# Kernel tuning notes

Hardware: AMD Instinct MI355X
Metric: run time of the kernel (lower is better)

Reference implementation:

```python
import jax, jax.numpy as jnp
import numpy as np

B, L, D = 4, 1024, 1024
N, H = 16, 64
FFW = 4096
LYR = 6
PDIM = 768            # 3 * 16^2
POS_EMB = 64
POOL_K = 4
EPS = 1e-6
BASE = 10000.0
GRID = 32             # 32x32 patch grid


def rms_norm(x, scale=None, eps=EPS):
    v = jnp.mean(jnp.square(x.astype(jnp.float32)), axis=-1, keepdims=True)
    y = (x.astype(jnp.float32) * jax.lax.rsqrt(v + eps)).astype(x.dtype)
    return y * scale if scale is not None else y


def _rope_half(x, pos, base):
    # x: [B, L, N, Hh]; pos: [B, L] int coords
    Hh = x.shape[-1]
    inv = 1.0 / (base ** (jnp.arange(Hh // 2, dtype=jnp.float32) / (Hh // 2)))
    ang = pos.astype(jnp.float32)[..., None] * inv          # [B, L, Hh/2]
    cos = jnp.cos(ang)[:, :, None, :]
    sin = jnp.sin(ang)[:, :, None, :]
    x1, x2 = jnp.split(x, 2, axis=-1)
    return jnp.concatenate([x1 * cos - x2 * sin, x2 * cos + x1 * sin], axis=-1)


def apply_2d_rope(x, px, py, base):
    # first half of head_dim rotated by x-coord, second half by y-coord
    xa, xb = jnp.split(x, 2, axis=-1)
    return jnp.concatenate([_rope_half(xa, px, base), _rope_half(xb, py, base)], axis=-1)


def setup_inputs() -> dict:
    key = jax.random.key(0)
    ks = jax.random.split(key, 12)
    pixel_values = jax.random.uniform(ks[0], (B, L, PDIM), dtype=jnp.float32)
    gx = jnp.arange(L, dtype=jnp.int32) % GRID
    gy = jnp.arange(L, dtype=jnp.int32) // GRID
    position_ids = jnp.broadcast_to(jnp.stack([gx, gy], -1), (B, L, 2))
    s = 0.02
    Win = jax.random.normal(ks[1], (PDIM, D), jnp.float32) * s
    pos_table = jax.random.normal(ks[2], (2, POS_EMB, D), jnp.float32) * s
    Wq = jax.random.normal(ks[3], (LYR, D, N * H), jnp.float32) * s
    Wk = jax.random.normal(ks[4], (LYR, D, N * H), jnp.float32) * s
    Wv = jax.random.normal(ks[5], (LYR, D, N * H), jnp.float32) * s
    Wo = jax.random.normal(ks[6], (LYR, N * H, D), jnp.float32) * s
    Wg = jax.random.normal(ks[7], (LYR, D, FFW), jnp.float32) * s
    Wu = jax.random.normal(ks[8], (LYR, D, FFW), jnp.float32) * s
    Wd = jax.random.normal(ks[9], (LYR, FFW, D), jnp.float32) * s
    qn = jnp.ones((LYR, H), jnp.float32)
    kn = jnp.ones((LYR, H), jnp.float32)
    pre_attn = jnp.ones((LYR, D), jnp.float32)
    post_attn = jnp.ones((LYR, D), jnp.float32)
    pre_ffw = jnp.ones((LYR, D), jnp.float32)
    post_ffw = jnp.ones((LYR, D), jnp.float32)
    return dict(pixel_values=pixel_values, position_ids=position_ids, Win=Win,
                pos_table=pos_table, Wq=Wq, Wk=Wk, Wv=Wv, Wo=Wo, qn=qn, kn=kn,
                pre_attn=pre_attn, post_attn=post_attn, pre_ffw=pre_ffw,
                post_ffw=post_ffw, Wg=Wg, Wu=Wu, Wd=Wd)


def _encoder(pixel_values, position_ids, Win, pos_table, Wq, Wk, Wv, Wo, qn, kn,
             pre_attn, post_attn, pre_ffw, post_ffw, Wg, Wu, Wd):
    padding = jnp.all(position_ids == -1, axis=-1)          # [B, L] True = pad
    valid = ~padding
    big_neg = jnp.finfo(jnp.float32).min
    amask = jnp.where((valid[:, :, None] & valid[:, None, :])[:, None], 0.0, big_neg)  # [B,1,L,L]

    px = position_ids[:, :, 0]
    py = position_ids[:, :, 1]
    clamped = jnp.maximum(position_ids, 0)

    # patch embed
    pix = 2.0 * (pixel_values - 0.5)
    x = pix @ Win
    pos_emb = pos_table[0][clamped[..., 0]] + pos_table[1][clamped[..., 1]]
    x = x + jnp.where(padding[..., None], 0.0, pos_emb)

    for i in range(LYR):
        # attention
        res = x
        h = rms_norm(x, pre_attn[i])
        q = (h @ Wq[i]).reshape(B, L, N, H)
        k = (h @ Wk[i]).reshape(B, L, N, H)
        v = (h @ Wv[i]).reshape(B, L, N, H)
        q = rms_norm(q, qn[i])
        k = rms_norm(k, kn[i])
        v = rms_norm(v)                                     # with_scale=False
        q = apply_2d_rope(q, px, py, BASE)
        k = apply_2d_rope(k, px, py, BASE)
        scores = jnp.einsum('bqnh,bknh->bnqk', q, k) + amask  # no 1/sqrt(H), matches source
        w = jax.nn.softmax(scores.astype(jnp.float32), axis=-1).astype(v.dtype)
        o = jnp.einsum('bnqk,bknh->bqnh', w, v).reshape(B, L, N * H) @ Wo[i]
        x = res + rms_norm(o, post_attn[i])
        # GeGLU MLP
        res = x
        h = rms_norm(x, pre_ffw[i])
        m = (jax.nn.gelu(h @ Wg[i], approximate=True) * (h @ Wu[i])) @ Wd[i]
        x = res + rms_norm(m, post_ffw[i])

    # pooler: 4x4 position-based average pooling
    out_len = L // (POOL_K ** 2)
    kk = int((L / out_len) ** 0.5)
    x = jnp.where(padding[..., None], 0.0, x)
    max_x = jnp.max(clamped[..., 0], axis=-1, keepdims=True) + 1   # [B,1]
    kidx = clamped // kk
    kidx = kidx[..., 0] + (max_x // kk) * kidx[..., 1]             # [B, L]
    weights = jax.nn.one_hot(kidx, out_len, dtype=jnp.float32) / (kk * kk)
    pooled = jnp.einsum('blo,bld->bod', weights, x.astype(jnp.float32))
    mask = jnp.any(weights != 0, axis=1)                           # [B, out_len]
    pooled = pooled.astype(x.dtype) * jnp.sqrt(jnp.float32(D))
    pooled = jnp.where(mask[..., None], pooled, 0.0)               # jit-safe stand-in for hidden[mask]
    return pooled, mask


def reference(pixel_values, position_ids, Win, pos_table, Wq, Wk, Wv, Wo, qn, kn,
              pre_attn, post_attn, pre_ffw, post_ffw, Wg, Wu, Wd):
    return _encoder(pixel_values, position_ids, Win, pos_table, Wq, Wk, Wv, Wo,
                    qn, kn, pre_attn, post_attn, pre_ffw, post_ffw, Wg, Wu, Wd)
```

## Files before the change

### kernel.cpp

```cpp
#include <hip/hip_runtime.h>
#include <stdint.h>

typedef unsigned short ushort_t;
using frag8 = __attribute__((ext_vector_type(8))) short;
using f32x4 = __attribute__((ext_vector_type(4))) float;

static __device__ __forceinline__ unsigned short f2bf(float f) {
  union { float f; unsigned u; } v; v.f = f;
  unsigned r = v.u + 0x7fffu + ((v.u >> 16) & 1u);
  return (unsigned short)(r >> 16);
}
static __device__ __forceinline__ float bf2f(unsigned short b) {
  union { unsigned u; float f; } v; v.u = ((unsigned)b) << 16; return v.f;
}
static __device__ __forceinline__ void splitf(float v, ushort_t& h, ushort_t& m) {
  h = f2bf(v);
  m = f2bf(v - bf2f(h));
}

__global__ __launch_bounds__(256) void k_splitpix(const float* __restrict__ pix,
                                                  ushort_t* __restrict__ oh,
                                                  ushort_t* __restrict__ om, int n4) {
  int i = blockIdx.x * 256 + threadIdx.x;
  if (i >= n4) return;
  float4 v = ((const float4*)pix)[i];
  ushort4 h, m;
  splitf(2.f * (v.x - 0.5f), h.x, m.x);
  splitf(2.f * (v.y - 0.5f), h.y, m.y);
  splitf(2.f * (v.z - 0.5f), h.z, m.z);
  splitf(2.f * (v.w - 0.5f), h.w, m.w);
  ((ushort4*)oh)[i] = h;
  ((ushort4*)om)[i] = m;
}

__global__ __launch_bounds__(256) void k_posemb(const int* __restrict__ pos,
                                                const float* __restrict__ ptab,
                                                float* __restrict__ x) {
  int row = blockIdx.x, tid = threadIdx.x;
  int p0 = pos[(size_t)row * 2], p1 = pos[(size_t)row * 2 + 1];
  bool pad = (p0 == -1) && (p1 == -1);
  int px = p0 > 0 ? p0 : 0, py = p1 > 0 ? p1 : 0;
  float4 a = ((const float4*)(ptab + (size_t)px * 1024))[tid];
  float4 b = ((const float4*)(ptab + 65536 + (size_t)py * 1024))[tid];
  float4 o;
  o.x = pad ? 0.f : a.x + b.x;
  o.y = pad ? 0.f : a.y + b.y;
  o.z = pad ? 0.f : a.z + b.z;
  o.w = pad ? 0.f : a.w + b.w;
  ((float4*)(x + (size_t)row * 1024))[tid] = o;
}

__global__ __launch_bounds__(256) void k_rmsnorm_s(const float* __restrict__ x,
                                                   const float* __restrict__ scale,
                                                   ushort_t* __restrict__ oh,
                                                   ushort_t* __restrict__ om) {
  __shared__ float wsum[4];
  int row = blockIdx.x, tid = threadIdx.x;
  float4 v = ((const float4*)(x + (size_t)row * 1024))[tid];
  float ss = v.x * v.x + v.y * v.y + v.z * v.z + v.w * v.w;
  for (int m = 1; m < 64; m <<= 1) ss += __shfl_xor(ss, m);
  if ((tid & 63) == 0) wsum[tid >> 6] = ss;
  __syncthreads();
  float tot = wsum[0] + wsum[1] + wsum[2] + wsum[3];
  float r = rsqrtf(tot * (1.f / 1024.f) + 1e-6f);
  float4 sc = ((const float4*)scale)[tid];
  ushort4 h, m;
  splitf(v.x * r * sc.x, h.x, m.x);
  splitf(v.y * r * sc.y, h.y, m.y);
  splitf(v.z * r * sc.z, h.z, m.z);
  splitf(v.w * r * sc.w, h.w, m.w);
  ((ushort4*)(oh + (size_t)row * 1024))[tid] = h;
  ((ushort4*)(om + (size_t)row * 1024))[tid] = m;
}

__global__ __launch_bounds__(256) void k_addrms32(float* __restrict__ x,
                                                  const float* __restrict__ t,
                                                  const float* __restrict__ scale) {
  __shared__ float wsum[4];
  int row = blockIdx.x, tid = threadIdx.x;
  float4 v = ((const float4*)(t + (size_t)row * 1024))[tid];
  float ss = v.x * v.x + v.y * v.y + v.z * v.z + v.w * v.w;
  for (int m = 1; m < 64; m <<= 1) ss += __shfl_xor(ss, m);
  if ((tid & 63) == 0) wsum[tid >> 6] = ss;
  __syncthreads();
  float tot = wsum[0] + wsum[1] + wsum[2] + wsum[3];
  float r = rsqrtf(tot * (1.f / 1024.f) + 1e-6f);
  float4 sc = ((const float4*)scale)[tid];
  float4 xv = ((const float4*)(x + (size_t)row * 1024))[tid];
  xv.x += v.x * r * sc.x;
  xv.y += v.y * r * sc.y;
  xv.z += v.z * r * sc.z;
  xv.w += v.w * r * sc.w;
  ((float4*)(x + (size_t)row * 1024))[tid] = xv;
}

__global__ __launch_bounds__(256) void k_qkv(const ushort_t* __restrict__ Ah,
                                             const ushort_t* __restrict__ Am,
                                             const float* __restrict__ Wq,
                                             const float* __restrict__ Wk,
                                             const float* __restrict__ Wv,
                                             const float* __restrict__ qn,
                                             const float* __restrict__ kn,
                                             const int* __restrict__ pos,
                                             ushort_t* __restrict__ qh, ushort_t* __restrict__ qm,
                                             ushort_t* __restrict__ kh, ushort_t* __restrict__ km,
                                             ushort_t* __restrict__ vh, ushort_t* __restrict__ vm) {
  __shared__ __align__(16) ushort_t Ash[128][40];
  __shared__ __align__(16) ushort_t Asl[128][40];
  __shared__ __align__(16) ushort_t Bsh[128][40];
  __shared__ __align__(16) ushort_t Bsl[128][40];
  const int tid = threadIdx.x;
  const int bid = blockIdx.x;
  const int xcd = bid & 7, lo = bid >> 3;
  const int ntl = lo % 3, mt = lo / 3;
  const int nt = xcd * 3 + ntl;
  const int mat = nt >> 3;
  const int n0 = (nt & 7) << 7;
  const int m0 = mt << 7;
  const float* B = (mat == 0) ? Wq : (mat == 1 ? Wk : Wv);

  const int lane = tid & 63;
  const int wm = ((tid >> 7) & 1) * 64;
  const int wn = ((tid >> 6) & 1) * 64;
  const int l15 = lane & 15, lg = lane >> 4;
  const int arow = tid >> 1, acol = (tid & 1) << 4;
  const int bnn = tid & 127, bk0 = (tid >> 7) << 4;
  f32x4 acc[4][4] = {};

  for (int k0 = 0; k0 < 1024; k0 += 32) {
    const ushort_t* gah = Ah + (size_t)(m0 + arow) * 1024 + (k0 + acol);
    const ushort_t* gam = Am + (size_t)(m0 + arow) * 1024 + (k0 + acol);
    uint4 a0 = *(const uint4*)gah;
    uint4 a1 = *(const uint4*)(gah + 8);
    uint4 a2 = *(const uint4*)gam;
    uint4 a3 = *(const uint4*)(gam + 8);
    const float* gb = B + (size_t)(k0 + bk0) * 1024 + (n0 + bnn);
    float bv[16];
#pragma unroll
    for (int j = 0; j < 16; ++j) bv[j] = gb[(size_t)j * 1024];
    *(uint4*)(&Ash[arow][acol]) = a0;
    *(uint4*)(&Ash[arow][acol + 8]) = a1;
    *(uint4*)(&Asl[arow][acol]) = a2;
    *(uint4*)(&Asl[arow][acol + 8]) = a3;
#pragma unroll
    for (int g = 0; g < 4; ++g) {
      ushort4 wh, wl;
      splitf(bv[g * 4 + 0], wh.x, wl.x);
      splitf(bv[g * 4 + 1], wh.y, wl.y);
      splitf(bv[g * 4 + 2], wh.z, wl.z);
      splitf(bv[g * 4 + 3], wh.w, wl.w);
      *(ushort4*)(&Bsh[bnn][bk0 + (g << 2)]) = wh;
      *(ushort4*)(&Bsl[bnn][bk0 + (g << 2)]) = wl;
    }
    __syncthreads();
    frag8 ah[4], al[4], bh[4], bl[4];
#pragma unroll
    for (int i = 0; i < 4; ++i) {
      ah[i] = *(const frag8*)(&Ash[wm + i * 16 + l15][lg << 3]);
      al[i] = *(const frag8*)(&Asl[wm + i * 16 + l15][lg << 3]);
      bh[i] = *(const frag8*)(&Bsh[wn + i * 16 + l15][lg << 3]);
      bl[i] = *(const frag8*)(&Bsl[wn + i * 16 + l15][lg << 3]);
    }
#pragma unroll
    for (int mi = 0; mi < 4; ++mi)
#pragma unroll
      for (int ni = 0; ni < 4; ++ni) {
        acc[mi][ni] = __builtin_amdgcn_mfma_f32_16x16x32_bf16(ah[mi], bh[ni], acc[mi][ni], 0, 0, 0);
        acc[mi][ni] = __builtin_amdgcn_mfma_f32_16x16x32_bf16(ah[mi], bl[ni], acc[mi][ni], 0, 0, 0);
        acc[mi][ni] = __builtin_amdgcn_mfma_f32_16x16x32_bf16(al[mi], bh[ni], acc[mi][ni], 0, 0, 0);
      }
    __syncthreads();
  }

  const float* scale = (mat == 0) ? qn : (mat == 1 ? kn : nullptr);
  ushort_t* outh = (mat == 0) ? qh : (mat == 1 ? kh : vh);
  ushort_t* outm = (mat == 0) ? qm : (mat == 1 ? km : vm);
  const float inv = powf(10000.f, -(float)l15 * (1.f / 16.f));
#pragma unroll
  for (int mi = 0; mi < 4; ++mi) {
#pragma unroll
    for (int rr = 0; rr < 4; ++rr) {
      float ss = 0.f;
#pragma unroll
      for (int ni = 0; ni < 4; ++ni) { float v = acc[mi][ni][rr]; ss += v * v; }
      ss += __shfl_xor(ss, 1);
      ss += __shfl_xor(ss, 2);
      ss += __shfl_xor(ss, 4);
      ss += __shfl_xor(ss, 8);
      float rs = rsqrtf(ss * (1.f / 64.f) + 1e-6f);
      int row = m0 + wm + mi * 16 + (lg << 2) + rr;
      float nv[4];
#pragma unroll
      for (int ni = 0; ni < 4; ++ni) {
        float sc = scale ? scale[ni * 16 + l15] : 1.f;
        nv[ni] = acc[mi][ni][rr] * rs * sc;
      }
      if (mat < 2) {
        int p0 = pos[(size_t)row * 2], p1 = pos[(size_t)row * 2 + 1];
        p0 = p0 > 0 ? p0 : 0;
        p1 = p1 > 0 ? p1 : 0;
        float a0 = (float)p0 * inv, a1 = (float)p1 * inv;
        float c0 = cosf(a0), s0 = sinf(a0);
        float c1 = cosf(a1), s1 = sinf(a1);
        float t0 = nv[0] * c0 - nv[1] * s0;
        float t1 = nv[1] * c0 + nv[0] * s0;
        float t2 = nv[2] * c1 - nv[3] * s1;
        float t3 = nv[3] * c1 + nv[2] * s1;
        nv[0] = t0; nv[1] = t1; nv[2] = t2; nv[3] = t3;
      }
#pragma unroll
      for (int ni = 0; ni < 4; ++ni) {
        ushort_t h, m;
        splitf(nv[ni], h, m);
        size_t idx = (size_t)row * 1024 + n0 + wn + ni * 16 + l15;
        outh[idx] = h;
        outm[idx] = m;
      }
    }
  }
}

__global__ __launch_bounds__(256) void k_ffw_up(const ushort_t* __restrict__ Ah,
                                                const ushort_t* __restrict__ Am,
                                                const float* __restrict__ Wg,
                                                const float* __restrict__ Wu,
                                                ushort_t* __restrict__ Oh,
                                                ushort_t* __restrict__ Om) {
  __shared__ __align__(16) ushort_t Ash[128][40];
  __shared__ __align__(16) ushort_t Asl[128][40];
  __shared__ __align__(16) ushort_t Bgh[128][40];
  __shared__ __align__(16) ushort_t Bgl[128][40];
  __shared__ __align__(16) ushort_t Buh[128][40];
  __shared__ __align__(16) ushort_t Bul[128][40];
  const int tid = threadIdx.x;
  const int bid = blockIdx.x;
  const int xcd = bid & 7, lo = bid >> 3;
  const int nt = xcd * 4 + (lo & 3);
  const int mt = lo >> 2;
  const int m0 = mt << 7, n0 = nt << 7;

  const int lane = tid & 63;
  const int wm = ((tid >> 7) & 1) * 64;
  const int wn = ((tid >> 6) & 1) * 64;
  const int l15 = lane & 15, lg = lane >> 4;
  const int arow = tid >> 1, acol = (tid & 1) << 4;
  const int bnn = tid & 127, bk0 = (tid >> 7) << 4;
  f32x4 ag[4][4] = {};
  f32x4 au[4][4] = {};

  for (int k0 = 0; k0 < 1024; k0 += 32) {
    const ushort_t* gah = Ah + (size_t)(m0 + arow) * 1024 + (k0 + acol);
    const ushort_t* gam = Am + (size_t)(m0 + arow) * 1024 + (k0 + acol);
    uint4 a0 = *(const uint4*)gah;
    uint4 a1 = *(const uint4*)(gah + 8);
    uint4 a2 = *(const uint4*)gam;
    uint4 a3 = *(const uint4*)(gam + 8);
    const float* gbg = Wg + (size_t)(k0 + bk0) * 4096 + (n0 + bnn);
    const float* gbu = Wu + (size_t)(k0 + bk0) * 4096 + (n0 + bnn);
    float bvg[16], bvu[16];
#pragma unroll
    for (int j = 0; j < 16; ++j) bvg[j] = gbg[(size_t)j * 4096];
#pragma unroll
    for (int j = 0; j < 16; ++j) bvu[j] = gbu[(size_t)j * 4096];
    *(uint4*)(&Ash[arow][acol]) = a0;
    *(uint4*)(&Ash[arow][acol + 8]) = a1;
    *(uint4*)(&Asl[arow][acol]) = a2;
    *(uint4*)(&Asl[arow][acol + 8]) = a3;
#pragma unroll
    for (int g = 0; g < 4; ++g) {
      ushort4 wh, wl;
      splitf(bvg[g * 4 + 0], wh.x, wl.x);
      splitf(bvg[g * 4 + 1], wh.y, wl.y);
      splitf(bvg[g * 4 + 2], wh.z, wl.z);
      splitf(bvg[g * 4 + 3], wh.w, wl.w);
      *(ushort4*)(&Bgh[bnn][bk0 + (g << 2)]) = wh;
      *(ushort4*)(&Bgl[bnn][bk0 + (g << 2)]) = wl;
      splitf(bvu[g * 4 + 0], wh.x, wl.x);
      splitf(bvu[g * 4 + 1], wh.y, wl.y);
      splitf(bvu[g * 4 + 2], wh.z, wl.z);
      splitf(bvu[g * 4 + 3], wh.w, wl.w);
      *(ushort4*)(&Buh[bnn][bk0 + (g << 2)]) = wh;
      *(ushort4*)(&Bul[bnn][bk0 + (g << 2)]) = wl;
    }
    __syncthreads();
    frag8 ah[4], al[4];
#pragma unroll
    for (int i = 0; i < 4; ++i) {
      ah[i] = *(const frag8*)(&Ash[wm + i * 16 + l15][lg << 3]);
      al[i] = *(const frag8*)(&Asl[wm + i * 16 + l15][lg << 3]);
    }
#pragma unroll
    for (int ni = 0; ni < 4; ++ni) {
      frag8 bgh = *(const frag8*)(&Bgh[wn + ni * 16 + l15][lg << 3]);
      frag8 bgl = *(const frag8*)(&Bgl[wn + ni * 16 + l15][lg << 3]);
      frag8 buh = *(const frag8*)(&Buh[wn + ni * 16 + l15][lg << 3]);
      frag8 bul = *(const frag8*)(&Bul[wn + ni * 16 + l15][lg << 3]);
#pragma unroll
      for (int mi = 0; mi < 4; ++mi) {
        ag[mi][ni] = __builtin_amdgcn_mfma_f32_16x16x32_bf16(ah[mi], bgh, ag[mi][ni], 0, 0, 0);
        ag[mi][ni] = __builtin_amdgcn_mfma_f32_16x16x32_bf16(ah[mi], bgl, ag[mi][ni], 0, 0, 0);
        ag[mi][ni] = __builtin_amdgcn_mfma_f32_16x16x32_bf16(al[mi], bgh, ag[mi][ni], 0, 0, 0);
        au[mi][ni] = __builtin_amdgcn_mfma_f32_16x16x32_bf16(ah[mi], buh, au[mi][ni], 0, 0, 0);
        au[mi][ni] = __builtin_amdgcn_mfma_f32_16x16x32_bf16(ah[mi], bul, au[mi][ni], 0, 0, 0);
        au[mi][ni] = __builtin_amdgcn_mfma_f32_16x16x32_bf16(al[mi], buh, au[mi][ni], 0, 0, 0);
      }
    }
    __syncthreads();
  }

#pragma unroll
  for (int mi = 0; mi < 4; ++mi) {
#pragma unroll
    for (int ni = 0; ni < 4; ++ni) {
#pragma unroll
      for (int r = 0; r < 4; ++r) {
        float vg = ag[mi][ni][r];
        float x3 = vg * vg * vg;
        float gel = 0.5f * vg * (1.f + tanhf(0.7978845608028654f * (vg + 0.044715f * x3)));
        float v2 = gel * au[mi][ni][r];
        int gr = m0 + wm + mi * 16 + (lg << 2) + r;
        int gc = n0 + wn + ni * 16 + l15;
        size_t idx = (size_t)gr * 4096 + gc;
        ushort_t h, m;
        splitf(v2, h, m);
        Oh[idx] = h;
        Om[idx] = m;
      }
    }
  }
}

enum { EPI_F32 = 0, EPI_ADDF32 = 1 };

template <int EPI>
__global__ __launch_bounds__(256) void k_gemm_s(const ushort_t* __restrict__ Ah,
                                                const ushort_t* __restrict__ Am,
                                                const float* __restrict__ B,
                                                float* Cf, int K, int N) {
  __shared__ __align__(16) ushort_t Ash[128][40];
  __shared__ __align__(16) ushort_t Asl[128][40];
  __shared__ __align__(16) ushort_t Bsh[128][40];
  __shared__ __align__(16) ushort_t Bsl[128][40];
  const int tid = threadIdx.x;
  const int bid = blockIdx.x;
  const int xcd = bid & 7, lo = bid >> 3;
  const int mt = xcd * 4 + (lo >> 3);
  const int nt = lo & 7;
  const int m0 = mt << 7, n0 = nt << 7;
  const int lane = tid & 63;
  const int wm = ((tid >> 7) & 1) * 64;
  const int wn = ((tid >> 6) & 1) * 64;
  const int l15 = lane & 15, lg = lane >> 4;
  const int arow = tid >> 1, acol = (tid & 1) << 4;
  const int bnn = tid & 127, bk0 = (tid >> 7) << 4;
  f32x4 acc[4][4] = {};

  for (int k0 = 0; k0 < K; k0 += 32) {
    const ushort_t* gah = Ah + (size_t)(m0 + arow) * K + (k0 + acol);
    const ushort_t* gam = Am + (size_t)(m0 + arow) * K + (k0 + acol);
    uint4 a0 = *(const uint4*)gah;
    uint4 a1 = *(const uint4*)(gah + 8);
    uint4 a2 = *(const uint4*)gam;
    uint4 a3 = *(const uint4*)(gam + 8);
    const float* gb = B + (size_t)(k0 + bk0) * N + (n0 + bnn);
    float bv[16];
#pragma unroll
    for (int j = 0; j < 16; ++j) bv[j] = gb[(size_t)j * N];
    *(uint4*)(&Ash[arow][acol]) = a0;
    *(uint4*)(&Ash[arow][acol + 8]) = a1;
    *(uint4*)(&Asl[arow][acol]) = a2;
    *(uint4*)(&Asl[arow][acol + 8]) = a3;
#pragma unroll
    for (int g = 0; g < 4; ++g) {
      ushort4 wh, wl;
      splitf(bv[g * 4 + 0], wh.x, wl.x);
      splitf(bv[g * 4 + 1], wh.y, wl.y);
      splitf(bv[g * 4 + 2], wh.z, wl.z);
      splitf(bv[g * 4 + 3], wh.w, wl.w);
      *(ushort4*)(&Bsh[bnn][bk0 + (g << 2)]) = wh;
      *(ushort4*)(&Bsl[bnn][bk0 + (g << 2)]) = wl;
    }
    __syncthreads();
    frag8 ah[4], al[4], bh[4], bl[4];
#pragma unroll
    for (int i = 0; i < 4; ++i) {
      ah[i] = *(const frag8*)(&Ash[wm + i * 16 + l15][lg << 3]);
      al[i] = *(const frag8*)(&Asl[wm + i * 16 + l15][lg << 3]);
      bh[i] = *(const frag8*)(&Bsh[wn + i * 16 + l15][lg << 3]);
      bl[i] = *(const frag8*)(&Bsl[wn + i * 16 + l15][lg << 3]);
    }
#pragma unroll
    for (int mi = 0; mi < 4; ++mi)
#pragma unroll
      for (int ni = 0; ni < 4; ++ni) {
        acc[mi][ni] = __builtin_amdgcn_mfma_f32_16x16x32_bf16(ah[mi], bh[ni], acc[mi][ni], 0, 0, 0);
        acc[mi][ni] = __builtin_amdgcn_mfma_f32_16x16x32_bf16(ah[mi], bl[ni], acc[mi][ni], 0, 0, 0);
        acc[mi][ni] = __builtin_amdgcn_mfma_f32_16x16x32_bf16(al[mi], bh[ni], acc[mi][ni], 0, 0, 0);
      }
    __syncthreads();
  }

#pragma unroll
  for (int mi = 0; mi < 4; ++mi) {
#pragma unroll
    for (int ni = 0; ni < 4; ++ni) {
#pragma unroll
      for (int r = 0; r < 4; ++r) {
        float val = acc[mi][ni][r];
        int gr = m0 + wm + mi * 16 + (lg << 2) + r;
        int gc = n0 + wn + ni * 16 + l15;
        size_t idx = (size_t)gr * N + gc;
        if (EPI == EPI_F32) Cf[idx] = val;
        else Cf[idx] += val;
      }
    }
  }
}

__global__ __launch_bounds__(256) void k_attn_s(const ushort_t* __restrict__ qh,
                                                const ushort_t* __restrict__ qm,
                                                const ushort_t* __restrict__ kh,
                                                const ushort_t* __restrict__ km,
                                                const ushort_t* __restrict__ vh,
                                                const ushort_t* __restrict__ vm,
                                                ushort_t* __restrict__ oh,
                                                ushort_t* __restrict__ om) {
  __shared__ __align__(16) ushort_t Khs[64][72];
  __shared__ __align__(16) ushort_t Kms[64][72];
  __shared__ __align__(16) ushort_t Vhs[64][72];
  __shared__ __align__(16) ushort_t Vms[64][72];
  __shared__ __align__(16) ushort_t Phs[64][72];
  __shared__ __align__(16) ushort_t Pms[64][72];
  const int tid = threadIdx.x;
  const int bid = blockIdx.x;
  const int xcd = bid & 7, lo = bid >> 3;
  const int bh_ = xcd * 8 + (lo >> 4);
  const int qt = lo & 15;
  const int b = bh_ >> 4, n = bh_ & 15;
  const size_t base = (size_t)b * 1048576 + (size_t)n * 64;
  const int lane = tid & 63, w = tid >> 6;
  const int l15 = lane & 15, lg = lane >> 4;

  {
    int row = tid >> 2, cg = (tid & 3) << 4;
    const uint4* sh = (const uint4*)(qh + base + (size_t)(qt * 64 + row) * 1024 + cg);
    const uint4* sm = (const uint4*)(qm + base + (size_t)(qt * 64 + row) * 1024 + cg);
    uint4 h0 = sh[0], h1 = sh[1], m0v = sm[0], m1v = sm[1];
    *(uint4*)(&Khs[row][cg]) = h0;
    *(uint4*)(&Khs[row][cg + 8]) = h1;
    *(uint4*)(&Kms[row][cg]) = m0v;
    *(uint4*)(&Kms[row][cg + 8]) = m1v;
  }
  __syncthreads();
  frag8 qh0 = *(const frag8*)(&Khs[w * 16 + l15][lg << 3]);
  frag8 qh1 = *(const frag8*)(&Khs[w * 16 + l15][32 + (lg << 3)]);
  frag8 qm0 = *(const frag8*)(&Kms[w * 16 + l15][lg << 3]);
  frag8 qm1 = *(const frag8*)(&Kms[w * 16 + l15][32 + (lg << 3)]);

  f32x4 oacc[4] = {};
  float mrun[4], srun[4];
#pragma unroll
  for (int r = 0; r < 4; ++r) { mrun[r] = -3.0e38f; srun[r] = 0.f; }

  for (int t = 0; t < 16; ++t) {
    __syncthreads();
    {
      int row = tid >> 2, cg = (tid & 3) << 4;
      const uint4* sh = (const uint4*)(kh + base + (size_t)(t * 64 + row) * 1024 + cg);
      const uint4* sm = (const uint4*)(km + base + (size_t)(t * 64 + row) * 1024 + cg);
      uint4 h0 = sh[0], h1 = sh[1], m0v = sm[0], m1v = sm[1];
      *(uint4*)(&Khs[row][cg]) = h0;
      *(uint4*)(&Khs[row][cg + 8]) = h1;
      *(uint4*)(&Kms[row][cg]) = m0v;
      *(uint4*)(&Kms[row][cg + 8]) = m1v;
    }
    {
      int hcol = tid & 63, kg = tid >> 6;
      ushort_t th[16], tm_[16];
#pragma unroll
      for (int j = 0; j < 16; ++j) {
        size_t off = base + (size_t)(t * 64 + kg * 16 + j) * 1024 + hcol;
        th[j] = vh[off];
        tm_[j] = vm[off];
      }
#pragma unroll
      for (int g = 0; g < 4; ++g) {
        ushort4 wv, wv2;
        wv.x = th[g * 4]; wv.y = th[g * 4 + 1]; wv.z = th[g * 4 + 2]; wv.w = th[g * 4 + 3];
        wv2.x = tm_[g * 4]; wv2.y = tm_[g * 4 + 1]; wv2.z = tm_[g * 4 + 2]; wv2.w = tm_[g * 4 + 3];
        *(ushort4*)(&Vhs[hcol][kg * 16 + g * 4]) = wv;
        *(ushort4*)(&Vms[hcol][kg * 16 + g * 4]) = wv2;
      }
    }
    __syncthreads();

    f32x4 sacc[4] = {};
#pragma unroll
    for (int nf = 0; nf < 4; ++nf) {
      frag8 kh0 = *(const frag8*)(&Khs[nf * 16 + l15][lg << 3]);
      frag8 kh1 = *(const frag8*)(&Khs[nf * 16 + l15][32 + (lg << 3)]);
      frag8 km0 = *(const frag8*)(&Kms[nf * 16 + l15][lg << 3]);
      frag8 km1 = *(const frag8*)(&Kms[nf * 16 + l15][32 + (lg << 3)]);
      sacc[nf] = __builtin_amdgcn_mfma_f32_16x16x32_bf16(qh0, kh0, sacc[nf], 0, 0, 0);
      sacc[nf] = __builtin_amdgcn_mfma_f32_16x16x32_bf16(qh1, kh1, sacc[nf], 0, 0, 0);
      sacc[nf] = __builtin_amdgcn_mfma_f32_16x16x32_bf16(qh0, km0, sacc[nf], 0, 0, 0);
      sacc[nf] = __builtin_amdgcn_mfma_f32_16x16x32_bf16(qh1, km1, sacc[nf], 0, 0, 0);
      sacc[nf] = __builtin_amdgcn_mfma_f32_16x16x32_bf16(qm0, kh0, sacc[nf], 0, 0, 0);
      sacc[nf] = __builtin_amdgcn_mfma_f32_16x16x32_bf16(qm1, kh1, sacc[nf], 0, 0, 0);
    }
#pragma unroll
    for (int r = 0; r < 4; ++r) {
      float tm = fmaxf(fmaxf(sacc[0][r], sacc[1][r]), fmaxf(sacc[2][r], sacc[3][r]));
      tm = fmaxf(tm, __shfl_xor(tm, 1));
      tm = fmaxf(tm, __shfl_xor(tm, 2));
      tm = fmaxf(tm, __shfl_xor(tm, 4));
      tm = fmaxf(tm, __shfl_xor(tm, 8));
      float nm = fmaxf(mrun[r], tm);
      float al = expf(mrun[r] - nm);
      float p0 = expf(sacc[0][r] - nm);
      float p1 = expf(sacc[1][r] - nm);
      float p2 = expf(sacc[2][r] - nm);
      float p3 = expf(sacc[3][r] - nm);
      float rs = p0 + p1 + p2 + p3;
      rs += __shfl_xor(rs, 1);
      rs += __shfl_xor(rs, 2);
      rs += __shfl_xor(rs, 4);
      rs += __shfl_xor(rs, 8);
      srun[r] = srun[r] * al + rs;
      mrun[r] = nm;
#pragma unroll
      for (int hf = 0; hf < 4; ++hf) oacc[hf][r] *= al;
      int prow = w * 16 + lg * 4 + r;
      ushort_t ph, pm;
      splitf(p0, ph, pm); Phs[prow][0 * 16 + l15] = ph; Pms[prow][0 * 16 + l15] = pm;
      splitf(p1, ph, pm); Phs[prow][1 * 16 + l15] = ph; Pms[prow][1 * 16 + l15] = pm;
      splitf(p2, ph, pm); Phs[prow][2 * 16 + l15] = ph; Pms[prow][2 * 16 + l15] = pm;
      splitf(p3, ph, pm); Phs[prow][3 * 16 + l15] = ph; Pms[prow][3 * 16 + l15] = pm;
    }
    __syncthreads();
#pragma unroll
    for (int kg = 0; kg < 2; ++kg) {
      frag8 pf = *(const frag8*)(&Phs[w * 16 + l15][kg * 32 + (lg << 3)]);
      frag8 pf2 = *(const frag8*)(&Pms[w * 16 + l15][kg * 32 + (lg << 3)]);
#pragma unroll
      for (int hf = 0; hf < 4; ++hf) {
        frag8 vf = *(const frag8*)(&Vhs[hf * 16 + l15][kg * 32 + (lg << 3)]);
        frag8 vf2 = *(const frag8*)(&Vms[hf * 16 + l15][kg * 32 + (lg << 3)]);
        oacc[hf] = __builtin_amdgcn_mfma_f32_16x16x32_bf16(pf, vf, oacc[hf], 0, 0, 0);
        oacc[hf] = __builtin_amdgcn_mfma_f32_16x16x32_bf16(pf, vf2, oacc[hf], 0, 0, 0);
        oacc[hf] = __builtin_amdgcn_mfma_f32_16x16x32_bf16(pf2, vf, oacc[hf], 0, 0, 0);
      }
    }
  }
#pragma unroll
  for (int hf = 0; hf < 4; ++hf)
#pragma unroll
    for (int r = 0; r < 4; ++r) {
      float val = oacc[hf][r] / srun[r];
      size_t off = base + (size_t)(qt * 64 + w * 16 + lg * 4 + r) * 1024 + hf * 16 + l15;
      ushort_t h, m;
      splitf(val, h, m);
      oh[off] = h;
      om[off] = m;
    }
}

__global__ __launch_bounds__(256) void k_pool(const float* __restrict__ x,
                                              const int* __restrict__ pos,
                                              float* __restrict__ out,
                                              float* __restrict__ maskout) {
  __shared__ int smax[4];
  __shared__ int kidx_s[1024];
  const int blk = blockIdx.x;
  const int b = blk >> 6, oidx = blk & 63;
  const int tid = threadIdx.x;
  int mx = 0;
  for (int l = tid; l < 1024; l += 256) {
    int p0 = pos[((size_t)b * 1024 + l) * 2];
    mx = max(mx, p0 > 0 ? p0 : 0);
  }
  for (int m = 1; m < 64; m <<= 1) mx = max(mx, __shfl_xor(mx, m));
  if ((tid & 63) == 0) smax[tid >> 6] = mx;
  __syncthreads();
  int maxx = max(max(smax[0], smax[1]), max(smax[2], smax[3])) + 1;
  int mk = maxx >> 2;
  for (int l = tid; l < 1024; l += 256) {
    int p0 = pos[((size_t)b * 1024 + l) * 2];
    int p1 = pos[((size_t)b * 1024 + l) * 2 + 1];
    int c0 = p0 > 0 ? p0 : 0, c1 = p1 > 0 ? p1 : 0;
    int pad = (p0 == -1 && p1 == -1) ? 1 : 0;
    kidx_s[l] = ((c0 >> 2) + mk * (c1 >> 2)) | (pad << 16);
  }
  __syncthreads();
  float ax = 0.f, ay = 0.f, az = 0.f, aw = 0.f;
  int cnt = 0;
  for (int l = 0; l < 1024; ++l) {
    int ki = kidx_s[l];
    if ((ki & 0xffff) == oidx) {
      cnt++;
      if (!(ki >> 16)) {
        float4 xv = ((const float4*)(x + ((size_t)b * 1024 + l) * 1024))[tid];
        ax += xv.x; ay += xv.y; az += xv.z; aw += xv.w;
      }
    }
  }
  float4 res;
  res.x = ax * 2.0f; res.y = ay * 2.0f; res.z = az * 2.0f; res.w = aw * 2.0f;
  ((float4*)(out + ((size_t)b * 64 + oidx) * 1024))[tid] = res;
  if (tid == 0) maskout[b * 64 + oidx] = (cnt > 0) ? 1.0f : 0.0f;
}

extern "C" void kernel_launch(void* const* d_in, const int* in_sizes, int n_in,
                              void* d_out, int out_size, void* d_ws, size_t ws_size,
                              hipStream_t stream) {
  const float* pix = (const float*)d_in[0];
  const int* pos = (const int*)d_in[1];
  const float* Win = (const float*)d_in[2];
  const float* ptab = (const float*)d_in[3];
  const float* Wq = (const float*)d_in[4];
  const float* Wk = (const float*)d_in[5];
  const float* Wv = (const float*)d_in[6];
  const float* Wo = (const float*)d_in[7];
  const float* qn = (const float*)d_in[8];
  const float* kn = (const float*)d_in[9];
  const float* pre_attn = (const float*)d_in[10];
  const float* post_attn = (const float*)d_in[11];
  const float* pre_ffw = (const float*)d_in[12];
  const float* post_ffw = (const float*)d_in[13];
  const float* Wg = (const float*)d_in[14];
  const float* Wu = (const float*)d_in[15];
  const float* Wd = (const float*)d_in[16];

  char* w = (char*)d_ws;
  float* x = (float*)w;        w += 16777216;
  float* tmp = (float*)w;      w += 16777216;
  ushort_t* hh = (ushort_t*)w; w += 8388608;
  ushort_t* hm = (ushort_t*)w; w += 8388608;
  char* regB = w;
  ushort_t* qh_ = (ushort_t*)(regB + 0);
  ushort_t* qm_ = (ushort_t*)(regB + 8388608);
  ushort_t* kh_ = (ushort_t*)(regB + 16777216);
  ushort_t* km_ = (ushort_t*)(regB + 25165824);
  ushort_t* vh_ = (ushort_t*)(regB + 33554432);
  ushort_t* vm_ = (ushort_t*)(regB + 41943040);
  ushort_t* aoh = (ushort_t*)(regB + 50331648);
  ushort_t* aom = (ushort_t*)(regB + 58720256);
  ushort_t* mh = (ushort_t*)(regB + 0);
  ushort_t* mm = (ushort_t*)(regB + 33554432);
  ushort_t* pixh = (ushort_t*)(regB + 0);
  ushort_t* pixm = (ushort_t*)(regB + 6291456);

  dim3 blk(256);
  k_splitpix<<<3072, blk, 0, stream>>>(pix, pixh, pixm, 786432);
  k_posemb<<<4096, blk, 0, stream>>>(pos, ptab, x);
  k_gemm_s<EPI_ADDF32><<<256, blk, 0, stream>>>(pixh, pixm, Win, x, 768, 1024);

  for (int i = 0; i < 6; ++i) {
    const float* wq = Wq + (size_t)i * 1048576;
    const float* wk = Wk + (size_t)i * 1048576;
    const float* wv = Wv + (size_t)i * 1048576;
    const float* wo = Wo + (size_t)i * 1048576;
    const float* wg = Wg + (size_t)i * 4194304;
    const float* wu = Wu + (size_t)i * 4194304;
    const float* wd = Wd + (size_t)i * 4194304;

    k_rmsnorm_s<<<4096, blk, 0, stream>>>(x, pre_attn + i * 1024, hh, hm);
    k_qkv<<<768, blk, 0, stream>>>(hh, hm, wq, wk, wv, qn + i * 64, kn + i * 64, pos,
                                   qh_, qm_, kh_, km_, vh_, vm_);
    k_attn_s<<<1024, blk, 0, stream>>>(qh_, qm_, kh_, km_, vh_, vm_, aoh, aom);
    k_gemm_s<EPI_F32><<<256, blk, 0, stream>>>(aoh, aom, wo, tmp, 1024, 1024);
    k_addrms32<<<4096, blk, 0, stream>>>(x, tmp, post_attn + i * 1024);

    k_rmsnorm_s<<<4096, blk, 0, stream>>>(x, pre_ffw + i * 1024, hh, hm);
    k_ffw_up<<<1024, blk, 0, stream>>>(hh, hm, wg, wu, mh, mm);
    k_gemm_s<EPI_F32><<<256, blk, 0, stream>>>(mh, mm, wd, tmp, 4096, 1024);
    k_addrms32<<<4096, blk, 0, stream>>>(x, tmp, post_ffw + i * 1024);
  }

  k_pool<<<256, blk, 0, stream>>>(x, pos, (float*)d_out, (float*)d_out + 262144);
}
```

Baseline: 5.560 ms.

## Pre-split weights into transposed bf16 hi/lo and load GEMM fragments directly

Adds a k_wsplit4 kernel that transposes each layer's fp32 weights once per call and splits them into bf16 high and low halves. Before, every M-tile block re-split the same weight tile on the fly. The QKV, FFW-up and generic GEMMs now read MFMA fragments straight from global memory, with no LDS staging and no barriers. This removes the redundant split arithmetic and the strided fp32 weight loads. In exchange it adds transpose-split passes with their own memory traffic and extra workspace, and the GEMMs lose LDS reuse and any prefetch pipelining, leaving global-load latency exposed.

```diff
diff --git a/kernel.cpp b/kernel.cpp
--- a/kernel.cpp
+++ b/kernel.cpp
@@ -31,6 +31,41 @@
   splitf(2.f * (v.w - 0.5f), h.w, m.w);
   ((ushort4*)oh)[i] = h;
   ((ushort4*)om)[i] = m;
+}
+
+__global__ __launch_bounds__(256) void k_wsplit4(const float* __restrict__ B0,
+                                                 const float* __restrict__ B1,
+                                                 const float* __restrict__ B2,
+                                                 const float* __restrict__ B3,
+                                                 ushort_t* __restrict__ th,
+                                                 ushort_t* __restrict__ tm,
+                                                 int K, int N) {
+  __shared__ float ts[64][65];
+  const int z = blockIdx.z;
+  const float* B = (z == 0) ? B0 : (z == 1) ? B1 : (z == 2) ? B2 : B3;
+  th += (size_t)z * K * N;
+  tm += (size_t)z * K * N;
+  const int tid = threadIdx.x;
+  const int n0 = blockIdx.x << 6, k0 = blockIdx.y << 6;
+  int rr = tid >> 4, cc = (tid & 15) << 2;
+#pragma unroll
+  for (int j = 0; j < 4; ++j) {
+    int r = rr + j * 16;
+    float4 v = *(const float4*)(B + (size_t)(k0 + r) * N + n0 + cc);
+    ts[r][cc] = v.x; ts[r][cc + 1] = v.y; ts[r][cc + 2] = v.z; ts[r][cc + 3] = v.w;
+  }
+  __syncthreads();
+  int n = tid >> 2;
+  int kc = (tid & 3) << 4;
+  ushort_t oh[16], om[16];
+#pragma unroll
+  for (int j = 0; j < 16; ++j) splitf(ts[kc + j][n], oh[j], om[j]);
+  ushort_t* ph = th + (size_t)(n0 + n) * K + k0 + kc;
+  ushort_t* pm = tm + (size_t)(n0 + n) * K + k0 + kc;
+  *(uint4*)(ph) = *(uint4*)(oh);
+  *(uint4*)(ph + 8) = *(uint4*)(oh + 8);
+  *(uint4*)(pm) = *(uint4*)(om);
+  *(uint4*)(pm + 8) = *(uint4*)(om + 8);
 }
 
 __global__ __launch_bounds__(256) void k_posemb(const int* __restrict__ pos,
@@ -96,19 +131,14 @@
 
 __global__ __launch_bounds__(256) void k_qkv(const ushort_t* __restrict__ Ah,
                                              const ushort_t* __restrict__ Am,
-                                             const float* __restrict__ Wq,
-                                             const float* __restrict__ Wk,
-                                             const float* __restrict__ Wv,
+                                             const ushort_t* __restrict__ WT_h,
+                                             const ushort_t* __restrict__ WT_m,
                                              const float* __restrict__ qn,
                                              const float* __restrict__ kn,
                                              const int* __restrict__ pos,
                                              ushort_t* __restrict__ qh, ushort_t* __restrict__ qm,
                                              ushort_t* __restrict__ kh, ushort_t* __restrict__ km,
                                              ushort_t* __restrict__ vh, ushort_t* __restrict__ vm) {
-  __shared__ __align__(16) ushort_t Ash[128][40];
-  __shared__ __align__(16) ushort_t Asl[128][40];
-  __shared__ __align__(16) ushort_t Bsh[128][40];
-  __shared__ __align__(16) ushort_t Bsl[128][40];
   const int tid = threadIdx.x;
   const int bid = blockIdx.x;
   const int xcd = bid & 7, lo = bid >> 3;
@@ -117,59 +147,39 @@
   const int mat = nt >> 3;
   const int n0 = (nt & 7) << 7;
   const int m0 = mt << 7;
-  const float* B = (mat == 0) ? Wq : (mat == 1 ? Wk : Wv);
+  const ushort_t* Bh = WT_h + (size_t)mat * 1048576;
+  const ushort_t* Bm = WT_m + (size_t)mat * 1048576;
 
   const int lane = tid & 63;
   const int wm = ((tid >> 7) & 1) * 64;
   const int wn = ((tid >> 6) & 1) * 64;
   const int l15 = lane & 15, lg = lane >> 4;
-  const int arow = tid >> 1, acol = (tid & 1) << 4;
-  const int bnn = tid & 127, bk0 = (tid >> 7) << 4;
   f32x4 acc[4][4] = {};
 
+  const ushort_t* pa_h = Ah + (size_t)(m0 + wm + l15) * 1024 + lg * 8;
+  const ushort_t* pa_m = Am + (size_t)(m0 + wm + l15) * 1024 + lg * 8;
+  const ushort_t* pb_h = Bh + (size_t)(n0 + wn + l15) * 1024 + lg * 8;
+  const ushort_t* pb_m = Bm + (size_t)(n0 + wn + l15) * 1024 + lg * 8;
+
+#pragma unroll 1
   for (int k0 = 0; k0 < 1024; k0 += 32) {
-    const ushort_t* gah = Ah + (size_t)(m0 + arow) * 1024 + (k0 + acol);
-    const ushort_t* gam = Am + (size_t)(m0 + arow) * 1024 + (k0 + acol);
-    uint4 a0 = *(const uint4*)gah;
-    uint4 a1 = *(const uint4*)(gah + 8);
-    uint4 a2 = *(const uint4*)gam;
-    uint4 a3 = *(const uint4*)(gam + 8);
-    const float* gb = B + (size_t)(k0 + bk0) * 1024 + (n0 + bnn);
-    float bv[16];
-#pragma unroll
-    for (int j = 0; j < 16; ++j) bv[j] = gb[(size_t)j * 1024];
-    *(uint4*)(&Ash[arow][acol]) = a0;
-    *(uint4*)(&Ash[arow][acol + 8]) = a1;
-    *(uint4*)(&Asl[arow][acol]) = a2;
-    *(uint4*)(&Asl[arow][acol + 8]) = a3;
-#pragma unroll
-    for (int g = 0; g < 4; ++g) {
-      ushort4 wh, wl;
-      splitf(bv[g * 4 + 0], wh.x, wl.x);
-      splitf(bv[g * 4 + 1], wh.y, wl.y);
-      splitf(bv[g * 4 + 2], wh.z, wl.z);
-      splitf(bv[g * 4 + 3], wh.w, wl.w);
-      *(ushort4*)(&Bsh[bnn][bk0 + (g << 2)]) = wh;
-      *(ushort4*)(&Bsl[bnn][bk0 + (g << 2)]) = wl;
-    }
-    __syncthreads();
-    frag8 ah[4], al[4], bh[4], bl[4];
+    frag8 ah[4], al[4];
 #pragma unroll
     for (int i = 0; i < 4; ++i) {
-      ah[i] = *(const frag8*)(&Ash[wm + i * 16 + l15][lg << 3]);
-      al[i] = *(const frag8*)(&Asl[wm + i * 16 + l15][lg << 3]);
-      bh[i] = *(const frag8*)(&Bsh[wn + i * 16 + l15][lg << 3]);
-      bl[i] = *(const frag8*)(&Bsl[wn + i * 16 + l15][lg << 3]);
-    }
-#pragma unroll
-    for (int mi = 0; mi < 4; ++mi)
-#pragma unroll
-      for (int ni = 0; ni < 4; ++ni) {
-        acc[mi][ni] = __builtin_amdgcn_mfma_f32_16x16x32_bf16(ah[mi], bh[ni], acc[mi][ni], 0, 0, 0);
-        acc[mi][ni] = __builtin_amdgcn_mfma_f32_16x16x32_bf16(ah[mi], bl[ni], acc[mi][ni], 0, 0, 0);
-        acc[mi][ni] = __builtin_amdgcn_mfma_f32_16x16x32_bf16(al[mi], bh[ni], acc[mi][ni], 0, 0, 0);
-      }
-    __syncthreads();
+      ah[i] = *(const frag8*)(pa_h + (size_t)i * 16 * 1024 + k0);
+      al[i] = *(const frag8*)(pa_m + (size_t)i * 16 * 1024 + k0);
+    }
+#pragma unroll
+    for (int ni = 0; ni < 4; ++ni) {
+      frag8 bh = *(const frag8*)(pb_h + (size_t)ni * 16 * 1024 + k0);
+      frag8 bl = *(const frag8*)(pb_m + (size_t)ni * 16 * 1024 + k0);
+#pragma unroll
+      for (int mi = 0; mi < 4; ++mi) {
+        acc[mi][ni] = __builtin_amdgcn_mfma_f32_16x16x32_bf16(ah[mi], bh, acc[mi][ni], 0, 0, 0);
+        acc[mi][ni] = __builtin_amdgcn_mfma_f32_16x16x32_bf16(ah[mi], bl, acc[mi][ni], 0, 0, 0);
+        acc[mi][ni] = __builtin_amdgcn_mfma_f32_16x16x32_bf16(al[mi], bh, acc[mi][ni], 0, 0, 0);
+      }
+    }
   }
 
   const float* scale = (mat == 0) ? qn : (mat == 1 ? kn : nullptr);
@@ -222,79 +232,46 @@
 
 __global__ __launch_bounds__(256) void k_ffw_up(const ushort_t* __restrict__ Ah,
                                                 const ushort_t* __restrict__ Am,
-                                                const float* __restrict__ Wg,
-                                                const float* __restrict__ Wu,
+                                                const ushort_t* __restrict__ Gh,
+                                                const ushort_t* __restrict__ Gm,
+                                                const ushort_t* __restrict__ Uh,
+                                                const ushort_t* __restrict__ Um,
                                                 ushort_t* __restrict__ Oh,
                                                 ushort_t* __restrict__ Om) {
-  __shared__ __align__(16) ushort_t Ash[128][40];
-  __shared__ __align__(16) ushort_t Asl[128][40];
-  __shared__ __align__(16) ushort_t Bgh[128][40];
-  __shared__ __align__(16) ushort_t Bgl[128][40];
-  __shared__ __align__(16) ushort_t Buh[128][40];
-  __shared__ __align__(16) ushort_t Bul[128][40];
   const int tid = threadIdx.x;
   const int bid = blockIdx.x;
   const int xcd = bid & 7, lo = bid >> 3;
   const int nt = xcd * 4 + (lo & 3);
   const int mt = lo >> 2;
   const int m0 = mt << 7, n0 = nt << 7;
-
   const int lane = tid & 63;
   const int wm = ((tid >> 7) & 1) * 64;
   const int wn = ((tid >> 6) & 1) * 64;
   const int l15 = lane & 15, lg = lane >> 4;
-  const int arow = tid >> 1, acol = (tid & 1) << 4;
-  const int bnn = tid & 127, bk0 = (tid >> 7) << 4;
   f32x4 ag[4][4] = {};
   f32x4 au[4][4] = {};
 
+  const ushort_t* pa_h = Ah + (size_t)(m0 + wm + l15) * 1024 + lg * 8;
+  const ushort_t* pa_m = Am + (size_t)(m0 + wm + l15) * 1024 + lg * 8;
+  const ushort_t* pg_h = Gh + (size_t)(n0 + wn + l15) * 1024 + lg * 8;
+  const ushort_t* pg_m = Gm + (size_t)(n0 + wn + l15) * 1024 + lg * 8;
+  const ushort_t* pu_h = Uh + (size_t)(n0 + wn + l15) * 1024 + lg * 8;
+  const ushort_t* pu_m = Um + (size_t)(n0 + wn + l15) * 1024 + lg * 8;
+
+#pragma unroll 1
   for (int k0 = 0; k0 < 1024; k0 += 32) {
-    const ushort_t* gah = Ah + (size_t)(m0 + arow) * 1024 + (k0 + acol);
-    const ushort_t* gam = Am + (size_t)(m0 + arow) * 1024 + (k0 + acol);
-    uint4 a0 = *(const uint4*)gah;
-    uint4 a1 = *(const uint4*)(gah + 8);
-    uint4 a2 = *(const uint4*)gam;
-    uint4 a3 = *(const uint4*)(gam + 8);
-    const float* gbg = Wg + (size_t)(k0 + bk0) * 4096 + (n0 + bnn);
-    const float* gbu = Wu + (size_t)(k0 + bk0) * 4096 + (n0 + bnn);
-    float bvg[16], bvu[16];
-#pragma unroll
-    for (int j = 0; j < 16; ++j) bvg[j] = gbg[(size_t)j * 4096];
-#pragma unroll
-    for (int j = 0; j < 16; ++j) bvu[j] = gbu[(size_t)j * 4096];
-    *(uint4*)(&Ash[arow][acol]) = a0;
-    *(uint4*)(&Ash[arow][acol + 8]) = a1;
-    *(uint4*)(&Asl[arow][acol]) = a2;
-    *(uint4*)(&Asl[arow][acol + 8]) = a3;
-#pragma unroll
-    for (int g = 0; g < 4; ++g) {
-      ushort4 wh, wl;
-      splitf(bvg[g * 4 + 0], wh.x, wl.x);
-      splitf(bvg[g * 4 + 1], wh.y, wl.y);
-      splitf(bvg[g * 4 + 2], wh.z, wl.z);
-      splitf(bvg[g * 4 + 3], wh.w, wl.w);
-      *(ushort4*)(&Bgh[bnn][bk0 + (g << 2)]) = wh;
-      *(ushort4*)(&Bgl[bnn][bk0 + (g << 2)]) = wl;
-      splitf(bvu[g * 4 + 0], wh.x, wl.x);
-      splitf(bvu[g * 4 + 1], wh.y, wl.y);
-      splitf(bvu[g * 4 + 2], wh.z, wl.z);
-      splitf(bvu[g * 4 + 3], wh.w, wl.w);
-      *(ushort4*)(&Buh[bnn][bk0 + (g << 2)]) = wh;
-      *(ushort4*)(&Bul[bnn][bk0 + (g << 2)]) = wl;
-    }
-    __syncthreads();
     frag8 ah[4], al[4];
 #pragma unroll
     for (int i = 0; i < 4; ++i) {
-      ah[i] = *(const frag8*)(&Ash[wm + i * 16 + l15][lg << 3]);
-      al[i] = *(const frag8*)(&Asl[wm + i * 16 + l15][lg << 3]);
+      ah[i] = *(const frag8*)(pa_h + (size_t)i * 16 * 1024 + k0);
+      al[i] = *(const frag8*)(pa_m + (size_t)i * 16 * 1024 + k0);
     }
 #pragma unroll
     for (int ni = 0; ni < 4; ++ni) {
-      frag8 bgh = *(const frag8*)(&Bgh[wn + ni * 16 + l15][lg << 3]);
-      frag8 bgl = *(const frag8*)(&Bgl[wn + ni * 16 + l15][lg << 3]);
-      frag8 buh = *(const frag8*)(&Buh[wn + ni * 16 + l15][lg << 3]);
-      frag8 bul = *(const frag8*)(&Bul[wn + ni * 16 + l15][lg << 3]);
+      frag8 bgh = *(const frag8*)(pg_h + (size_t)ni * 16 * 1024 + k0);
+      frag8 bgl = *(const frag8*)(pg_m + (size_t)ni * 16 * 1024 + k0);
+      frag8 buh = *(const frag8*)(pu_h + (size_t)ni * 16 * 1024 + k0);
+      frag8 bul = *(const frag8*)(pu_m + (size_t)ni * 16 * 1024 + k0);
 #pragma unroll
       for (int mi = 0; mi < 4; ++mi) {
         ag[mi][ni] = __builtin_amdgcn_mfma_f32_16x16x32_bf16(ah[mi], bgh, ag[mi][ni], 0, 0, 0);
@@ -305,7 +282,6 @@
         au[mi][ni] = __builtin_amdgcn_mfma_f32_16x16x32_bf16(al[mi], buh, au[mi][ni], 0, 0, 0);
       }
     }
-    __syncthreads();
   }
 
 #pragma unroll
@@ -335,12 +311,9 @@
 template <int EPI>
 __global__ __launch_bounds__(256) void k_gemm_s(const ushort_t* __restrict__ Ah,
                                                 const ushort_t* __restrict__ Am,
-                                                const float* __restrict__ B,
+                                                const ushort_t* __restrict__ Bh,
+                                                const ushort_t* __restrict__ Bm,
                                                 float* Cf, int K, int N) {
-  __shared__ __align__(16) ushort_t Ash[128][40];
-  __shared__ __align__(16) ushort_t Asl[128][40];
-  __shared__ __align__(16) ushort_t Bsh[128][40];
-  __shared__ __align__(16) ushort_t Bsl[128][40];
   const int tid = threadIdx.x;
   const int bid = blockIdx.x;
   const int xcd = bid & 7, lo = bid >> 3;
@@ -351,53 +324,32 @@
   const int wm = ((tid >> 7) & 1) * 64;
   const int wn = ((tid >> 6) & 1) * 64;
   const int l15 = lane & 15, lg = lane >> 4;
-  const int arow = tid >> 1, acol = (tid & 1) << 4;
-  const int bnn = tid & 127, bk0 = (tid >> 7) << 4;
   f32x4 acc[4][4] = {};
 
+  const ushort_t* pa_h = Ah + (size_t)(m0 + wm + l15) * K + lg * 8;
+  const ushort_t* pa_m = Am + (size_t)(m0 + wm + l15) * K + lg * 8;
+  const ushort_t* pb_h = Bh + (size_t)(n0 + wn + l15) * K + lg * 8;
+  const ushort_t* pb_m = Bm + (size_t)(n0 + wn + l15) * K + lg * 8;
+
+#pragma unroll 1
   for (int k0 = 0; k0 < K; k0 += 32) {
-    const ushort_t* gah = Ah + (size_t)(m0 + arow) * K + (k0 + acol);
-    const ushort_t* gam = Am + (size_t)(m0 + arow) * K + (k0 + acol);
-    uint4 a0 = *(const uint4*)gah;
-    uint4 a1 = *(const uint4*)(gah + 8);
-    uint4 a2 = *(const uint4*)gam;
-    uint4 a3 = *(const uint4*)(gam + 8);
-    const float* gb = B + (size_t)(k0 + bk0) * N + (n0 + bnn);
-    float bv[16];
-#pragma unroll
-    for (int j = 0; j < 16; ++j) bv[j] = gb[(size_t)j * N];
-    *(uint4*)(&Ash[arow][acol]) = a0;
-    *(uint4*)(&Ash[arow][acol + 8]) = a1;
-    *(uint4*)(&Asl[arow][acol]) = a2;
-    *(uint4*)(&Asl[arow][acol + 8]) = a3;
-#pragma unroll
-    for (int g = 0; g < 4; ++g) {
-      ushort4 wh, wl;
-      splitf(bv[g * 4 + 0], wh.x, wl.x);
-      splitf(bv[g * 4 + 1], wh.y, wl.y);
-      splitf(bv[g * 4 + 2], wh.z, wl.z);
-      splitf(bv[g * 4 + 3], wh.w, wl.w);
-      *(ushort4*)(&Bsh[bnn][bk0 + (g << 2)]) = wh;
-      *(ushort4*)(&Bsl[bnn][bk0 + (g << 2)]) = wl;
-    }
-    __syncthreads();
-    frag8 ah[4], al[4], bh[4], bl[4];
+    frag8 ah[4], al[4];
 #pragma unroll
     for (int i = 0; i < 4; ++i) {
-      ah[i] = *(const frag8*)(&Ash[wm + i * 16 + l15][lg << 3]);
-      al[i] = *(const frag8*)(&Asl[wm + i * 16 + l15][lg << 3]);
-      bh[i] = *(const frag8*)(&Bsh[wn + i * 16 + l15][lg << 3]);
-      bl[i] = *(const frag8*)(&Bsl[wn + i * 16 + l15][lg << 3]);
-    }
-#pragma unroll
-    for (int mi = 0; mi < 4; ++mi)
-#pragma unroll
-      for (int ni = 0; ni < 4; ++ni) {
-        acc[mi][ni] = __builtin_amdgcn_mfma_f32_16x16x32_bf16(ah[mi], bh[ni], acc[mi][ni], 0, 0, 0);
-        acc[mi][ni] = __builtin_amdgcn_mfma_f32_16x16x32_bf16(ah[mi], bl[ni], acc[mi][ni], 0, 0, 0);
-        acc[mi][ni] = __builtin_amdgcn_mfma_f32_16x16x32_bf16(al[mi], bh[ni], acc[mi][ni], 0, 0, 0);
-      }
-    __syncthreads();
+      ah[i] = *(const frag8*)(pa_h + (size_t)i * 16 * K + k0);
+      al[i] = *(const frag8*)(pa_m + (size_t)i * 16 * K + k0);
+    }
+#pragma unroll
+    for (int ni = 0; ni < 4; ++ni) {
+      frag8 bh = *(const frag8*)(pb_h + (size_t)ni * 16 * K + k0);
+      frag8 bl = *(const frag8*)(pb_m + (size_t)ni * 16 * K + k0);
+#pragma unroll
+      for (int mi = 0; mi < 4; ++mi) {
+        acc[mi][ni] = __builtin_amdgcn_mfma_f32_16x16x32_bf16(ah[mi], bh, acc[mi][ni], 0, 0, 0);
+        acc[mi][ni] = __builtin_amdgcn_mfma_f32_16x16x32_bf16(ah[mi], bl, acc[mi][ni], 0, 0, 0);
+        acc[mi][ni] = __builtin_amdgcn_mfma_f32_16x16x32_bf16(al[mi], bh, acc[mi][ni], 0, 0, 0);
+      }
+    }
   }
 
 #pragma unroll
@@ -645,15 +597,24 @@
   ushort_t* vm_ = (ushort_t*)(regB + 41943040);
   ushort_t* aoh = (ushort_t*)(regB + 50331648);
   ushort_t* aom = (ushort_t*)(regB + 58720256);
+  ushort_t* wat_h = (ushort_t*)(regB + 67108864);
+  ushort_t* wat_m = (ushort_t*)(regB + 75497472);
   ushort_t* mh = (ushort_t*)(regB + 0);
   ushort_t* mm = (ushort_t*)(regB + 33554432);
+  ushort_t* wgu_h = (ushort_t*)(regB + 67108864);
+  ushort_t* wgu_m = (ushort_t*)(regB + 83886080);
+  ushort_t* wd_h = (ushort_t*)(regB + 100663296);
+  ushort_t* wd_m = (ushort_t*)(regB + 109051904);
   ushort_t* pixh = (ushort_t*)(regB + 0);
   ushort_t* pixm = (ushort_t*)(regB + 6291456);
+  ushort_t* win_h = (ushort_t*)(regB + 67108864);
+  ushort_t* win_m = (ushort_t*)(regB + 71303168);
 
   dim3 blk(256);
   k_splitpix<<<3072, blk, 0, stream>>>(pix, pixh, pixm, 786432);
   k_posemb<<<4096, blk, 0, stream>>>(pos, ptab, x);
-  k_gemm_s<EPI_ADDF32><<<256, blk, 0, stream>>>(pixh, pixm, Win, x, 768, 1024);
+  k_wsplit4<<<dim3(16, 12, 1), blk, 0, stream>>>(Win, Win, Win, Win, win_h, win_m, 768, 1024);
+  k_gemm_s<EPI_ADDF32><<<256, blk, 0, stream>>>(pixh, pixm, win_h, win_m, x, 768, 1024);
 
   for (int i = 0; i < 6; ++i) {
     const float* wq = Wq + (size_t)i * 1048576;
@@ -665,15 +626,20 @@
     const float* wd = Wd + (size_t)i * 4194304;
 
     k_rmsnorm_s<<<4096, blk, 0, stream>>>(x, pre_attn + i * 1024, hh, hm);
-    k_qkv<<<768, blk, 0, stream>>>(hh, hm, wq, wk, wv, qn + i * 64, kn + i * 64, pos,
+    k_wsplit4<<<dim3(16, 16, 4), blk, 0, stream>>>(wq, wk, wv, wo, wat_h, wat_m, 1024, 1024);
+    k_qkv<<<768, blk, 0, stream>>>(hh, hm, wat_h, wat_m, qn + i * 64, kn + i * 64, pos,
                                    qh_, qm_, kh_, km_, vh_, vm_);
     k_attn_s<<<1024, blk, 0, stream>>>(qh_, qm_, kh_, km_, vh_, vm_, aoh, aom);
-    k_gemm_s<EPI_F32><<<256, blk, 0, stream>>>(aoh, aom, wo, tmp, 1024, 1024);
+    k_gemm_s<EPI_F32><<<256, blk, 0, stream>>>(aoh, aom, wat_h + 3145728, wat_m + 3145728,
+                                               tmp, 1024, 1024);
     k_addrms32<<<4096, blk, 0, stream>>>(x, tmp, post_attn + i * 1024);
 
     k_rmsnorm_s<<<4096, blk, 0, stream>>>(x, pre_ffw + i * 1024, hh, hm);
-    k_ffw_up<<<1024, blk, 0, stream>>>(hh, hm, wg, wu, mh, mm);
-    k_gemm_s<EPI_F32><<<256, blk, 0, stream>>>(mh, mm, wd, tmp, 4096, 1024);
+    k_wsplit4<<<dim3(64, 16, 2), blk, 0, stream>>>(wg, wu, wg, wu, wgu_h, wgu_m, 1024, 4096);
+    k_wsplit4<<<dim3(16, 64, 1), blk, 0, stream>>>(wd, wd, wd, wd, wd_h, wd_m, 4096, 1024);
+    k_ffw_up<<<1024, blk, 0, stream>>>(hh, hm, wgu_h, wgu_m, wgu_h + 4194304, wgu_m + 4194304,
+                                       mh, mm);
+    k_gemm_s<EPI_F32><<<256, blk, 0, stream>>>(mh, mm, wd_h, wd_m, tmp, 4096, 1024);
     k_addrms32<<<4096, blk, 0, stream>>>(x, tmp, post_ffw + i * 1024);
   }
 
```

Result: slower. 7.387 ms (+32.9%).
